# Performance work log

Measured on AMD Instinct MI355X. Metric: run time of the kernel, lower is better.

Reference implementation:

```python
import jax, jax.numpy as jnp
import numpy as np

N, E = 50000, 800000
F_IN, HID, OUT, H = 128, 32, 4, 8
NEG_SLOPE = 0.2


def gat_conv(x, src, dst, W, a_src, a_dst, b):
    """PyG GATConv (concat=True, eval mode). x: [N,Fin]; src/dst: [E'] (self-loops included).
    W: [Fin, Hh*C]; a_src/a_dst: [Hh, C]; b: [Hh*C]."""
    n = x.shape[0]
    Hh, C = a_src.shape
    h = (x @ W).reshape(n, Hh, C)                      # [N,H,C]
    alpha_src = jnp.einsum('nhc,hc->nh', h, a_src)     # [N,H]
    alpha_dst = jnp.einsum('nhc,hc->nh', h, a_dst)     # [N,H]
    alpha = jax.nn.leaky_relu(alpha_src[src] + alpha_dst[dst], NEG_SLOPE)  # [E',H]
    # segment softmax over incoming edges of each dst node
    amax = jax.ops.segment_max(alpha, dst, num_segments=n)  # [N,H]
    ex = jnp.exp(alpha - amax[dst])
    denom = jax.ops.segment_sum(ex, dst, num_segments=n)    # [N,H]
    w = ex / (denom[dst] + 1e-16)                            # [E',H]
    msg = h[src] * w[:, :, None]                             # [E',H,C]
    out = jax.ops.segment_sum(msg, dst, num_segments=n)     # [N,H,C]
    return out.reshape(n, Hh * C) + b


def setup_inputs() -> dict:
    key = jax.random.key(0)
    ks = jax.random.split(key, 9)
    x = jax.random.normal(ks[0], (N, F_IN), jnp.float32)
    # random edge list without self loops (PyG GATConv removes then re-adds self loops)
    rng = np.random.default_rng(0)
    s = rng.integers(0, N, size=E)
    d = rng.integers(0, N, size=E)
    d = np.where(d == s, (d + 1) % N, d)
    edge_index = jnp.asarray(np.stack([s, d]), dtype=jnp.int32)
    g = lambda k, shape, fan: jax.random.normal(k, shape, jnp.float32) * (1.0 / np.sqrt(fan))
    W1 = g(ks[1], (F_IN, H * HID), F_IN)
    a_src1 = g(ks[2], (H, HID), HID)
    a_dst1 = g(ks[3], (H, HID), HID)
    b1 = jnp.zeros((H * HID,), jnp.float32)
    W2 = g(ks[4], (H * HID, H * OUT), H * HID)
    a_src2 = g(ks[5], (H, OUT), OUT)
    a_dst2 = g(ks[6], (H, OUT), OUT)
    b2 = jnp.zeros((H * OUT,), jnp.float32)
    return {"x": x, "edge_index": edge_index, "W1": W1, "a_src1": a_src1,
            "a_dst1": a_dst1, "b1": b1, "W2": W2, "a_src2": a_src2,
            "a_dst2": a_dst2, "b2": b2}


def reference(x, edge_index, W1, a_src1, a_dst1, b1, W2, a_src2, a_dst2, b2):
    n = x.shape[0]
    loops = jnp.arange(n, dtype=edge_index.dtype)
    src = jnp.concatenate([edge_index[0], loops])
    dst = jnp.concatenate([edge_index[1], loops])
    # layer 1 (dropout_edge / dropout are no-ops in eval mode)
    h = gat_conv(x, src, dst, W1, a_src1, a_dst1, b1)
    h = jax.nn.leaky_relu(h, NEG_SLOPE)
    # final layer (concat=True per the original code) -> [N, OUT*H]
    out = gat_conv(h, src, dst, W2, a_src2, a_dst2, b2)
    return out
```

## Files before the change

kernel.cpp:

```cpp
#include <hip/hip_runtime.h>
#include <hip/hip_bf16.h>
#include <cstdint>
#include <cstddef>


__device__ __forceinline__ float lrelu(float a) { return a > 0.f ? a : 0.2f * a; }

__device__ __forceinline__ unsigned short f2bf(float f) {
  unsigned u = __float_as_uint(f);
  unsigned r = (u + 0x7fff + ((u >> 16) & 1)) >> 16;
  return (unsigned short)r;
}
__device__ __forceinline__ float bf_lo(unsigned q) { return __uint_as_float(q << 16); }
__device__ __forceinline__ float bf_hi(unsigned q) { return __uint_as_float(q & 0xffff0000u); }

typedef __attribute__((ext_vector_type(8))) short bf16x8;
typedef __attribute__((ext_vector_type(4))) float f32x4;

#define ROWCAP 64
#define CSTRIDE 16


__global__ __launch_bounds__(256) void k_scatter(const int* __restrict__ srce,
                                                 const int* __restrict__ dste, int E, int n,
                                                 int* __restrict__ cursor,
                                                 int* __restrict__ srcs,
                                                 const float* __restrict__ W1,
                                                 unsigned short* __restrict__ W1T,
                                                 const float* __restrict__ W2,
                                                 unsigned short* __restrict__ W2T,
                                                 const float* __restrict__ as1,
                                                 const float* __restrict__ ad1,
                                                 const float* __restrict__ as2,
                                                 const float* __restrict__ ad2,
                                                 unsigned short* __restrict__ Wa1T,
                                                 unsigned short* __restrict__ Wa2T) {
  int t = blockIdx.x * 256 + threadIdx.x;
  if (t < E + n) {
    int s, d;
    if (t < E) { s = srce[t]; d = dste[t]; } else { s = d = t - E; }
    int pos = atomicAdd(&cursor[d << 4], 1);
    srcs[(d << 6) + pos] = s;
  }
  if (t < 32768) {
    int k = t >> 8;
    int nn = t & 255;
    W1T[nn * 128 + k] = f2bf(W1[k * 256 + nn]);
  }
  if (t < 8192) {
    int k = t >> 5;
    int nn = t & 31;
    W2T[nn * 256 + k] = f2bf(W2[k * 32 + nn]);
  }
  if (t < 2048) {
    int j = t >> 7;
    int k = t & 127;
    const float* av = (j < 8) ? &as1[j * 32] : &ad1[(j - 8) * 32];
    const float* wv = &W1[k * 256 + (j & 7) * 32];
    float s = 0.f;
#pragma unroll
    for (int c = 0; c < 32; c++) s += wv[c] * av[c];
    Wa1T[j * 128 + k] = f2bf(s);
  }
  if (t < 4096) {
    int j = t >> 8;
    int k = t & 255;
    const float* av = (j < 8) ? &as2[j * 4] : &ad2[(j - 8) * 4];
    const float* wv = &W2[k * 32 + (j & 7) * 4];
    float s = 0.f;
#pragma unroll
    for (int c = 0; c < 4; c++) s += wv[c] * av[c];
    Wa2T[j * 256 + k] = f2bf(s);
  }
}


__global__ __launch_bounds__(256) void gemm1_mfma(const float* __restrict__ X,
                                                  const unsigned short* __restrict__ WT,
                                                  const unsigned short* __restrict__ WaT,
                                                  unsigned short* __restrict__ h1,
                                                  float* __restrict__ a_s1,
                                                  float* __restrict__ a_d1,
                                                  int M) {
  __shared__ unsigned short As[64 * 136];
  __shared__ unsigned short Bs[256 * 72];
  __shared__ unsigned short Was[16 * 72];
  const int row0 = blockIdx.x * 64;
  const int tid = threadIdx.x;
  const int wv = tid >> 6, lane = tid & 63;
  const int quad = lane >> 4, l15 = lane & 15;
  const int colw = wv * 64;

#pragma unroll
  for (int i = 0; i < 8; i++) {
    int j = tid + 256 * i;
    int r = j >> 5;
    int c4 = (j & 31) * 4;
    float4 v = make_float4(0.f, 0.f, 0.f, 0.f);
    if (row0 + r < M) v = *(const float4*)&X[(size_t)(row0 + r) * 128 + c4];
    uint2 p;
    p.x = (unsigned)f2bf(v.x) | ((unsigned)f2bf(v.y) << 16);
    p.y = (unsigned)f2bf(v.z) | ((unsigned)f2bf(v.w) << 16);
    *(uint2*)&As[r * 136 + c4] = p;
  }

  f32x4 acc[16];
#pragma unroll
  for (int i = 0; i < 16; i++) acc[i] = (f32x4)0.f;
  f32x4 acca = (f32x4)0.f;

  for (int kc = 0; kc < 128; kc += 64) {
    __syncthreads();
#pragma unroll
    for (int i = 0; i < 8; i++) {
      int j = tid + 256 * i;
      int nn = j >> 3;
      int kg = (j & 7) * 8;
      *(uint4*)&Bs[nn * 72 + kg] = *(const uint4*)&WT[nn * 128 + kc + kg];
    }
    if (tid < 128) {
      int j = tid >> 3;
      int kg = (tid & 7) * 8;
      *(uint4*)&Was[j * 72 + kg] = *(const uint4*)&WaT[j * 128 + kc + kg];
    }
    __syncthreads();
#pragma unroll
    for (int ks = 0; ks < 64; ks += 32) {
      bf16x8 af[4], bfr[4];
#pragma unroll
      for (int mi = 0; mi < 4; mi++)
        af[mi] = *(const bf16x8*)&As[(mi * 16 + l15) * 136 + kc + ks + quad * 8];
#pragma unroll
      for (int ni = 0; ni < 4; ni++)
        bfr[ni] = *(const bf16x8*)&Bs[(colw + ni * 16 + l15) * 72 + ks + quad * 8];
#pragma unroll
      for (int mi = 0; mi < 4; mi++)
#pragma unroll
        for (int ni = 0; ni < 4; ni++)
          acc[mi * 4 + ni] = __builtin_amdgcn_mfma_f32_16x16x32_bf16(
              af[mi], bfr[ni], acc[mi * 4 + ni], 0, 0, 0);
      bf16x8 afa = *(const bf16x8*)&As[(wv * 16 + l15) * 136 + kc + ks + quad * 8];
      bf16x8 bfa = *(const bf16x8*)&Was[l15 * 72 + ks + quad * 8];
      acca = __builtin_amdgcn_mfma_f32_16x16x32_bf16(afa, bfa, acca, 0, 0, 0);
    }
  }

#pragma unroll
  for (int mi = 0; mi < 4; mi++) {
#pragma unroll
    for (int r = 0; r < 4; r++) {
      int m = row0 + mi * 16 + quad * 4 + r;
      if (m < M) {
#pragma unroll
        for (int ni = 0; ni < 4; ni++)
          h1[(size_t)m * 256 + colw + ni * 16 + l15] = f2bf(acc[mi * 4 + ni][r]);
      }
    }
  }
#pragma unroll
  for (int r = 0; r < 4; r++) {
    int m = row0 + wv * 16 + quad * 4 + r;
    if (m < M) {
      if (l15 < 8) a_s1[m * 8 + l15] = acca[r];
      else         a_d1[m * 8 + (l15 - 8)] = acca[r];
    }
  }
}


__global__ __launch_bounds__(256) void gemm2_mfma(const unsigned short* __restrict__ Xb,
                                                  const unsigned short* __restrict__ W2T,
                                                  const unsigned short* __restrict__ WaT,
                                                  unsigned short* __restrict__ h2,
                                                  float* __restrict__ a_s2,
                                                  float* __restrict__ a_d2, int M) {
  __shared__ unsigned short As[64 * 264];
  __shared__ unsigned short Bs[32 * 264];
  __shared__ unsigned short Was[16 * 264];
  const int row0 = blockIdx.x * 64;
  const int tid = threadIdx.x;
  const int wv = tid >> 6, lane = tid & 63;
  const int quad = lane >> 4, l15 = lane & 15;

#pragma unroll
  for (int i = 0; i < 8; i++) {
    int j = tid + 256 * i;
    int r = j >> 5;
    int c8 = (j & 31) * 8;
    uint4 v = make_uint4(0, 0, 0, 0);
    if (row0 + r < M) v = *(const uint4*)&Xb[(size_t)(row0 + r) * 256 + c8];
    *(uint4*)&As[r * 264 + c8] = v;
  }
#pragma unroll
  for (int i = 0; i < 4; i++) {
    int j = tid + 256 * i;
    int nn = j >> 5;
    int kg = (j & 31) * 8;
    *(uint4*)&Bs[nn * 264 + kg] = *(const uint4*)&W2T[nn * 256 + kg];
  }
#pragma unroll
  for (int i = 0; i < 2; i++) {
    int j = tid + 256 * i;
    int nn = j >> 5;
    int kg = (j & 31) * 8;
    *(uint4*)&Was[nn * 264 + kg] = *(const uint4*)&WaT[nn * 256 + kg];
  }
  __syncthreads();

  f32x4 acc[2];
  acc[0] = (f32x4)0.f;
  acc[1] = (f32x4)0.f;
  f32x4 acca = (f32x4)0.f;
  const int mr = wv * 16;
#pragma unroll
  for (int ks = 0; ks < 256; ks += 32) {
    bf16x8 af = *(const bf16x8*)&As[(mr + l15) * 264 + ks + quad * 8];
    bf16x8 b0 = *(const bf16x8*)&Bs[(l15) * 264 + ks + quad * 8];
    bf16x8 b1 = *(const bf16x8*)&Bs[(16 + l15) * 264 + ks + quad * 8];
    bf16x8 ba = *(const bf16x8*)&Was[(l15) * 264 + ks + quad * 8];
    acc[0] = __builtin_amdgcn_mfma_f32_16x16x32_bf16(af, b0, acc[0], 0, 0, 0);
    acc[1] = __builtin_amdgcn_mfma_f32_16x16x32_bf16(af, b1, acc[1], 0, 0, 0);
    acca   = __builtin_amdgcn_mfma_f32_16x16x32_bf16(af, ba, acca, 0, 0, 0);
  }

#pragma unroll
  for (int r = 0; r < 4; r++) {
    int m = row0 + mr + quad * 4 + r;
    if (m < M) {
      h2[(size_t)m * 32 + l15]      = f2bf(acc[0][r]);
      h2[(size_t)m * 32 + 16 + l15] = f2bf(acc[1][r]);
      if (l15 < 8) a_s2[m * 8 + l15] = acca[r];
      else         a_d2[m * 8 + (l15 - 8)] = acca[r];
    }
  }
}


__global__ __launch_bounds__(256) void gat_agg_l1(const unsigned short* __restrict__ h,
                                                  const float* __restrict__ asrc,
                                                  const float* __restrict__ adst,
                                                  const int* __restrict__ rowcnt,
                                                  const int* __restrict__ srcs,
                                                  const float* __restrict__ bias,
                                                  unsigned short* __restrict__ out, int n) {
  int wave = threadIdx.x >> 6;
  int lane = threadIdx.x & 63;
  int d = blockIdx.x * 4 + wave;
  if (d >= n) return;
  d = __builtin_amdgcn_readfirstlane(d);
  const int cnt = __builtin_amdgcn_readfirstlane(rowcnt[d << 4]);
  const int* __restrict__ row = srcs + (d << 6);
  const int myhead = lane >> 3;
  float ad = adst[d * 8 + myhead];

  float denom = 0.f;
  float4 acc0 = make_float4(0.f, 0.f, 0.f, 0.f);
  float4 acc1 = make_float4(0.f, 0.f, 0.f, 0.f);
#define ACCA(ff, qq)                                        \
    acc0.x = fmaf(ff, bf_lo(qq.x), acc0.x);                 \
    acc0.y = fmaf(ff, bf_hi(qq.x), acc0.y);                 \
    acc0.z = fmaf(ff, bf_lo(qq.y), acc0.z);                 \
    acc0.w = fmaf(ff, bf_hi(qq.y), acc0.w);
#define ACCB(ff, qq)                                        \
    acc1.x = fmaf(ff, bf_lo(qq.x), acc1.x);                 \
    acc1.y = fmaf(ff, bf_hi(qq.x), acc1.y);                 \
    acc1.z = fmaf(ff, bf_lo(qq.y), acc1.z);                 \
    acc1.w = fmaf(ff, bf_hi(qq.y), acc1.w);

  for (int e = 0; e < cnt; e += 12) {
    int s[12];
#pragma unroll
    for (int j = 0; j < 12; j++) {
      int ee = e + j;
      s[j] = __builtin_amdgcn_readfirstlane(row[ee < cnt ? ee : cnt - 1]);
    }
    uint2 q[12];
#pragma unroll
    for (int j = 0; j < 12; j++)
      q[j] = *(const uint2*)&h[(size_t)s[j] * 256 + lane * 4];
    float av[12];
#pragma unroll
    for (int j = 0; j < 12; j++) av[j] = asrc[s[j] * 8 + myhead];
#pragma unroll
    for (int j = 0; j < 12; j += 2) {
      float w0 = (e + j     < cnt) ? __expf(lrelu(av[j]     + ad)) : 0.f;
      float w1 = (e + j + 1 < cnt) ? __expf(lrelu(av[j + 1] + ad)) : 0.f;
      denom += w0 + w1;
      ACCA(w0, q[j])
      ACCB(w1, q[j + 1])
    }
  }
#undef ACCA
#undef ACCB
  float4 acc;
  acc.x = acc0.x + acc1.x;
  acc.y = acc0.y + acc1.y;
  acc.z = acc0.z + acc1.z;
  acc.w = acc0.w + acc1.w;
  float inv = 1.f / (denom + 1e-16f);
  int f = lane * 4;
  float4 bv = *(const float4*)&bias[f];
  float rx = lrelu(acc.x * inv + bv.x);
  float ry = lrelu(acc.y * inv + bv.y);
  float rz = lrelu(acc.z * inv + bv.z);
  float rw = lrelu(acc.w * inv + bv.w);
  uint2 p;
  p.x = (unsigned)f2bf(rx) | ((unsigned)f2bf(ry) << 16);
  p.y = (unsigned)f2bf(rz) | ((unsigned)f2bf(rw) << 16);
  *(uint2*)&out[(size_t)d * 256 + f] = p;
}

__global__ __launch_bounds__(256) void gat_agg_l2(const unsigned short* __restrict__ h,
                                                  const float* __restrict__ asrc,
                                                  const float* __restrict__ adst,
                                                  const int* __restrict__ rowcnt,
                                                  const int* __restrict__ srcs,
                                                  const float* __restrict__ bias,
                                                  float* __restrict__ out, int n) {
  int wave = threadIdx.x >> 6;
  int lane = threadIdx.x & 63;
  int d = blockIdx.x * 4 + wave;
  if (d >= n) return;
  int begin = d << 6;
  int end = begin + rowcnt[d << 4];
  int hh = lane & 7;
  int eg = lane >> 3;
  float ad = adst[d * 8 + hh];

  float denom = 0.f;
  float4 acc = make_float4(0.f, 0.f, 0.f, 0.f);
  for (int base = begin; base < end; base += 32) {
    int eA = base + eg;
    int eB = base + 8 + eg;
    int eC = base + 16 + eg;
    int eD = base + 24 + eg;
    bool vA = eA < end, vB = eB < end, vC = eC < end, vD = eD < end;
    int sA = srcs[vA ? eA : begin];
    int sB = srcs[vB ? eB : begin];
    int sC = srcs[vC ? eC : begin];
    int sD = srcs[vD ? eD : begin];
    float aA = asrc[sA * 8 + hh];
    float aB = asrc[sB * 8 + hh];
    float aC = asrc[sC * 8 + hh];
    float aD = asrc[sD * 8 + hh];
    uint2 qA = *(const uint2*)&h[(size_t)sA * 32 + hh * 4];
    uint2 qB = *(const uint2*)&h[(size_t)sB * 32 + hh * 4];
    uint2 qC = *(const uint2*)&h[(size_t)sC * 32 + hh * 4];
    uint2 qD = *(const uint2*)&h[(size_t)sD * 32 + hh * 4];
    float wA = vA ? __expf(lrelu(aA + ad)) : 0.f;
    float wB = vB ? __expf(lrelu(aB + ad)) : 0.f;
    float wC = vC ? __expf(lrelu(aC + ad)) : 0.f;
    float wD = vD ? __expf(lrelu(aD + ad)) : 0.f;
    denom += (wA + wB) + (wC + wD);
    acc.x = fmaf(wA, bf_lo(qA.x), acc.x); acc.y = fmaf(wA, bf_hi(qA.x), acc.y);
    acc.z = fmaf(wA, bf_lo(qA.y), acc.z); acc.w = fmaf(wA, bf_hi(qA.y), acc.w);
    acc.x = fmaf(wB, bf_lo(qB.x), acc.x); acc.y = fmaf(wB, bf_hi(qB.x), acc.y);
    acc.z = fmaf(wB, bf_lo(qB.y), acc.z); acc.w = fmaf(wB, bf_hi(qB.y), acc.w);
    acc.x = fmaf(wC, bf_lo(qC.x), acc.x); acc.y = fmaf(wC, bf_hi(qC.x), acc.y);
    acc.z = fmaf(wC, bf_lo(qC.y), acc.z); acc.w = fmaf(wC, bf_hi(qC.y), acc.w);
    acc.x = fmaf(wD, bf_lo(qD.x), acc.x); acc.y = fmaf(wD, bf_hi(qD.x), acc.y);
    acc.z = fmaf(wD, bf_lo(qD.y), acc.z); acc.w = fmaf(wD, bf_hi(qD.y), acc.w);
  }
#pragma unroll
  for (int mask = 8; mask <= 32; mask <<= 1) {
    denom += __shfl_xor(denom, mask);
    acc.x += __shfl_xor(acc.x, mask);
    acc.y += __shfl_xor(acc.y, mask);
    acc.z += __shfl_xor(acc.z, mask);
    acc.w += __shfl_xor(acc.w, mask);
  }
  if (lane < 8) {
    float inv = 1.f / (denom + 1e-16f);
    int f = lane * 4;
    float4 bv = *(const float4*)&bias[f];
    float4 r;
    r.x = acc.x * inv + bv.x;
    r.y = acc.y * inv + bv.y;
    r.z = acc.z * inv + bv.z;
    r.w = acc.w * inv + bv.w;
    *(float4*)&out[(size_t)d * 32 + f] = r;
  }
}


extern "C" void kernel_launch(void* const* d_in, const int* in_sizes, int n_in,
                              void* d_out, int out_size, void* d_ws, size_t ws_size,
                              hipStream_t stream) {
  const float* x   = (const float*)d_in[0];
  const int*   ei  = (const int*)d_in[1];
  const float* W1  = (const float*)d_in[2];
  const float* as1 = (const float*)d_in[3];
  const float* ad1 = (const float*)d_in[4];
  const float* b1  = (const float*)d_in[5];
  const float* W2  = (const float*)d_in[6];
  const float* as2 = (const float*)d_in[7];
  const float* ad2 = (const float*)d_in[8];
  const float* b2  = (const float*)d_in[9];
  float* out = (float*)d_out;

  const int E = in_sizes[1] / 2;
  const int n = in_sizes[0] / 128;
  const int* srce = ei;
  const int* dste = ei + E;

  char* ws = (char*)d_ws;
  size_t off = 0;
  auto alloc = [&](size_t bytes) -> void* {
    void* p = ws + off;
    off = (off + bytes + 255) & ~(size_t)255;
    return p;
  };
  int* cursor   = (int*)alloc((size_t)n * CSTRIDE * 4);
  int* srcs     = (int*)alloc((size_t)n * ROWCAP * 4);
  unsigned short* h1  = (unsigned short*)alloc((size_t)n * 256 * 2);
  unsigned short* w1t = (unsigned short*)alloc((size_t)256 * 128 * 2);
  unsigned short* w2t = (unsigned short*)alloc((size_t)32 * 256 * 2);
  unsigned short* wa1t = (unsigned short*)alloc((size_t)16 * 128 * 2);
  unsigned short* wa2t = (unsigned short*)alloc((size_t)16 * 256 * 2);
  float* a_s1   = (float*)alloc((size_t)n * 8 * 4);
  float* a_d1   = (float*)alloc((size_t)n * 8 * 4);
  unsigned short* x2 = (unsigned short*)alloc((size_t)n * 256 * 2);
  unsigned short* h2 = (unsigned short*)alloc((size_t)n * 32 * 2);
  float* a_s2   = (float*)alloc((size_t)n * 8 * 4);
  float* a_d2   = (float*)alloc((size_t)n * 8 * 4);

  const int tot = E + n;
  hipMemsetAsync(cursor, 0, (size_t)n * CSTRIDE * 4, stream);
  k_scatter<<<(tot + 255) / 256, 256, 0, stream>>>(srce, dste, E, n, cursor, srcs,
                                                   W1, w1t, W2, w2t,
                                                   as1, ad1, as2, ad2, wa1t, wa2t);

  gemm1_mfma<<<(n + 63) / 64, 256, 0, stream>>>(x, w1t, wa1t, h1, a_s1, a_d1, n);
  gat_agg_l1<<<(n + 3) / 4, 256, 0, stream>>>(h1, a_s1, a_d1, cursor, srcs, b1, x2, n);

  gemm2_mfma<<<(n + 63) / 64, 256, 0, stream>>>(x2, w2t, wa2t, h2, a_s2, a_d2, n);
  gat_agg_l2<<<(n + 3) / 4, 256, 0, stream>>>(h2, a_s2, a_d2, cursor, srcs, b2, out, n);
}
```

Baseline: 258.3 us.

## Pre-convert X to bf16 in scatter kernel and read weights directly in gemm1

Moves the fp32-to-bf16 conversion of the input features into the existing scatter/prep kernel, so gemm1 loads compact bf16 rows. gemm1 also drops its shared-memory staging of the weight and attention-projection matrices and reads MFMA B fragments directly from global memory, removing the K-loop barriers and most LDS usage. The trade-off is an extra write and read of the bf16 copy of X, plus relying on cache for the repeated weight fragment loads.

```diff
diff --git a/kernel.cpp b/kernel.cpp
--- a/kernel.cpp
+++ b/kernel.cpp
@@ -25,6 +25,8 @@
                                                  const int* __restrict__ dste, int E, int n,
                                                  int* __restrict__ cursor,
                                                  int* __restrict__ srcs,
+                                                 const float* __restrict__ X,
+                                                 unsigned short* __restrict__ Xb,
                                                  const float* __restrict__ W1,
                                                  unsigned short* __restrict__ W1T,
                                                  const float* __restrict__ W2,
@@ -36,6 +38,21 @@
                                                  unsigned short* __restrict__ Wa1T,
                                                  unsigned short* __restrict__ Wa2T) {
   int t = blockIdx.x * 256 + threadIdx.x;
+
+  {
+    size_t base = (size_t)t * 8;
+    if (base < (size_t)n * 128) {
+      float4 v0 = *(const float4*)&X[base];
+      float4 v1 = *(const float4*)&X[base + 4];
+      uint4 p;
+      p.x = (unsigned)f2bf(v0.x) | ((unsigned)f2bf(v0.y) << 16);
+      p.y = (unsigned)f2bf(v0.z) | ((unsigned)f2bf(v0.w) << 16);
+      p.z = (unsigned)f2bf(v1.x) | ((unsigned)f2bf(v1.y) << 16);
+      p.w = (unsigned)f2bf(v1.z) | ((unsigned)f2bf(v1.w) << 16);
+      *(uint4*)&Xb[base] = p;
+    }
+  }
+
   if (t < E + n) {
     int s, d;
     if (t < E) { s = srce[t]; d = dste[t]; } else { s = d = t - E; }
@@ -75,7 +92,7 @@
 }
 
 
-__global__ __launch_bounds__(256) void gemm1_mfma(const float* __restrict__ X,
+__global__ __launch_bounds__(256) void gemm1_mfma(const unsigned short* __restrict__ Xb,
                                                   const unsigned short* __restrict__ WT,
                                                   const unsigned short* __restrict__ WaT,
                                                   unsigned short* __restrict__ h1,
@@ -83,8 +100,6 @@
                                                   float* __restrict__ a_d1,
                                                   int M) {
   __shared__ unsigned short As[64 * 136];
-  __shared__ unsigned short Bs[256 * 72];
-  __shared__ unsigned short Was[16 * 72];
   const int row0 = blockIdx.x * 64;
   const int tid = threadIdx.x;
   const int wv = tid >> 6, lane = tid & 63;
@@ -92,57 +107,39 @@
   const int colw = wv * 64;
 
 #pragma unroll
-  for (int i = 0; i < 8; i++) {
+  for (int i = 0; i < 4; i++) {
     int j = tid + 256 * i;
-    int r = j >> 5;
-    int c4 = (j & 31) * 4;
-    float4 v = make_float4(0.f, 0.f, 0.f, 0.f);
-    if (row0 + r < M) v = *(const float4*)&X[(size_t)(row0 + r) * 128 + c4];
-    uint2 p;
-    p.x = (unsigned)f2bf(v.x) | ((unsigned)f2bf(v.y) << 16);
-    p.y = (unsigned)f2bf(v.z) | ((unsigned)f2bf(v.w) << 16);
-    *(uint2*)&As[r * 136 + c4] = p;
-  }
+    int r = j >> 4;
+    int c8 = (j & 15) * 8;
+    uint4 v = make_uint4(0, 0, 0, 0);
+    if (row0 + r < M) v = *(const uint4*)&Xb[(size_t)(row0 + r) * 128 + c8];
+    *(uint4*)&As[r * 136 + c8] = v;
+  }
+  __syncthreads();
 
   f32x4 acc[16];
 #pragma unroll
   for (int i = 0; i < 16; i++) acc[i] = (f32x4)0.f;
   f32x4 acca = (f32x4)0.f;
 
-  for (int kc = 0; kc < 128; kc += 64) {
-    __syncthreads();
-#pragma unroll
-    for (int i = 0; i < 8; i++) {
-      int j = tid + 256 * i;
-      int nn = j >> 3;
-      int kg = (j & 7) * 8;
-      *(uint4*)&Bs[nn * 72 + kg] = *(const uint4*)&WT[nn * 128 + kc + kg];
-    }
-    if (tid < 128) {
-      int j = tid >> 3;
-      int kg = (tid & 7) * 8;
-      *(uint4*)&Was[j * 72 + kg] = *(const uint4*)&WaT[j * 128 + kc + kg];
-    }
-    __syncthreads();
-#pragma unroll
-    for (int ks = 0; ks < 64; ks += 32) {
-      bf16x8 af[4], bfr[4];
-#pragma unroll
-      for (int mi = 0; mi < 4; mi++)
-        af[mi] = *(const bf16x8*)&As[(mi * 16 + l15) * 136 + kc + ks + quad * 8];
+#pragma unroll
+  for (int ks = 0; ks < 128; ks += 32) {
+    bf16x8 af[4], bfr[4];
+#pragma unroll
+    for (int mi = 0; mi < 4; mi++)
+      af[mi] = *(const bf16x8*)&As[(mi * 16 + l15) * 136 + ks + quad * 8];
+#pragma unroll
+    for (int ni = 0; ni < 4; ni++)
+      bfr[ni] = *(const bf16x8*)&WT[(size_t)(colw + ni * 16 + l15) * 128 + ks + quad * 8];
+#pragma unroll
+    for (int mi = 0; mi < 4; mi++)
 #pragma unroll
       for (int ni = 0; ni < 4; ni++)
-        bfr[ni] = *(const bf16x8*)&Bs[(colw + ni * 16 + l15) * 72 + ks + quad * 8];
-#pragma unroll
-      for (int mi = 0; mi < 4; mi++)
-#pragma unroll
-        for (int ni = 0; ni < 4; ni++)
-          acc[mi * 4 + ni] = __builtin_amdgcn_mfma_f32_16x16x32_bf16(
-              af[mi], bfr[ni], acc[mi * 4 + ni], 0, 0, 0);
-      bf16x8 afa = *(const bf16x8*)&As[(wv * 16 + l15) * 136 + kc + ks + quad * 8];
-      bf16x8 bfa = *(const bf16x8*)&Was[l15 * 72 + ks + quad * 8];
-      acca = __builtin_amdgcn_mfma_f32_16x16x32_bf16(afa, bfa, acca, 0, 0, 0);
-    }
+        acc[mi * 4 + ni] = __builtin_amdgcn_mfma_f32_16x16x32_bf16(
+            af[mi], bfr[ni], acc[mi * 4 + ni], 0, 0, 0);
+    bf16x8 afa = *(const bf16x8*)&As[(wv * 16 + l15) * 136 + ks + quad * 8];
+    bf16x8 bfa = *(const bf16x8*)&WaT[l15 * 128 + ks + quad * 8];
+    acca = __builtin_amdgcn_mfma_f32_16x16x32_bf16(afa, bfa, acca, 0, 0, 0);
   }
 
 #pragma unroll
@@ -412,6 +409,7 @@
   };
   int* cursor   = (int*)alloc((size_t)n * CSTRIDE * 4);
   int* srcs     = (int*)alloc((size_t)n * ROWCAP * 4);
+  unsigned short* xb  = (unsigned short*)alloc((size_t)n * 128 * 2);
   unsigned short* h1  = (unsigned short*)alloc((size_t)n * 256 * 2);
   unsigned short* w1t = (unsigned short*)alloc((size_t)256 * 128 * 2);
   unsigned short* w2t = (unsigned short*)alloc((size_t)32 * 256 * 2);
@@ -427,10 +425,10 @@
   const int tot = E + n;
   hipMemsetAsync(cursor, 0, (size_t)n * CSTRIDE * 4, stream);
   k_scatter<<<(tot + 255) / 256, 256, 0, stream>>>(srce, dste, E, n, cursor, srcs,
-                                                   W1, w1t, W2, w2t,
+                                                   x, xb, W1, w1t, W2, w2t,
                                                    as1, ad1, as2, ad2, wa1t, wa2t);
 
-  gemm1_mfma<<<(n + 63) / 64, 256, 0, stream>>>(x, w1t, wa1t, h1, a_s1, a_d1, n);
+  gemm1_mfma<<<(n + 63) / 64, 256, 0, stream>>>(xb, w1t, wa1t, h1, a_s1, a_d1, n);
   gat_agg_l1<<<(n + 3) / 4, 256, 0, stream>>>(h1, a_s1, a_d1, cursor, srcs, b1, x2, n);
 
   gemm2_mfma<<<(n + 63) / 64, 256, 0, stream>>>(x2, w2t, wa2t, h2, a_s2, a_d2, n);
```

Result: no change. 258.3 us (-0.0%).

## Fuse edge scatter into GEMM1 launch and read weights directly from global

Applied to the files above, without the earlier changes.

The edge-bucketing scatter moves out of the weight-prep kernel into extra blocks of the first GEMM launch, so the atomic-heavy scatter and the MFMA GEMM can run concurrently on different CUs. Weight transposition now runs in a small separate prep kernel of 128 blocks. The GEMM also drops its LDS staging of the weight tiles and loads B fragments straight from global memory (L2-resident), which removes the extra syncs and LDS traffic. The cost is an additional kernel launch and uncoalesced, repeated global loads of the weights.

```diff
diff --git a/kernel.cpp b/kernel.cpp
--- a/kernel.cpp
+++ b/kernel.cpp
@@ -21,27 +21,17 @@
 #define CSTRIDE 16
 
 
-__global__ __launch_bounds__(256) void k_scatter(const int* __restrict__ srce,
-                                                 const int* __restrict__ dste, int E, int n,
-                                                 int* __restrict__ cursor,
-                                                 int* __restrict__ srcs,
-                                                 const float* __restrict__ W1,
-                                                 unsigned short* __restrict__ W1T,
-                                                 const float* __restrict__ W2,
-                                                 unsigned short* __restrict__ W2T,
-                                                 const float* __restrict__ as1,
-                                                 const float* __restrict__ ad1,
-                                                 const float* __restrict__ as2,
-                                                 const float* __restrict__ ad2,
-                                                 unsigned short* __restrict__ Wa1T,
-                                                 unsigned short* __restrict__ Wa2T) {
+__global__ __launch_bounds__(256) void k_prep(const float* __restrict__ W1,
+                                              unsigned short* __restrict__ W1T,
+                                              const float* __restrict__ W2,
+                                              unsigned short* __restrict__ W2T,
+                                              const float* __restrict__ as1,
+                                              const float* __restrict__ ad1,
+                                              const float* __restrict__ as2,
+                                              const float* __restrict__ ad2,
+                                              unsigned short* __restrict__ Wa1T,
+                                              unsigned short* __restrict__ Wa2T) {
   int t = blockIdx.x * 256 + threadIdx.x;
-  if (t < E + n) {
-    int s, d;
-    if (t < E) { s = srce[t]; d = dste[t]; } else { s = d = t - E; }
-    int pos = atomicAdd(&cursor[d << 4], 1);
-    srcs[(d << 6) + pos] = s;
-  }
   if (t < 32768) {
     int k = t >> 8;
     int nn = t & 255;
@@ -75,17 +65,32 @@
 }
 
 
-__global__ __launch_bounds__(256) void gemm1_mfma(const float* __restrict__ X,
-                                                  const unsigned short* __restrict__ WT,
-                                                  const unsigned short* __restrict__ WaT,
-                                                  unsigned short* __restrict__ h1,
-                                                  float* __restrict__ a_s1,
-                                                  float* __restrict__ a_d1,
-                                                  int M) {
+__global__ __launch_bounds__(256) void fused_front(const float* __restrict__ X,
+                                                   const unsigned short* __restrict__ WT,
+                                                   const unsigned short* __restrict__ WaT,
+                                                   unsigned short* __restrict__ h1,
+                                                   float* __restrict__ a_s1,
+                                                   float* __restrict__ a_d1,
+                                                   int M,
+                                                   const int* __restrict__ srce,
+                                                   const int* __restrict__ dste, int E,
+                                                   int* __restrict__ cursor,
+                                                   int* __restrict__ srcs,
+                                                   int SB) {
   __shared__ unsigned short As[64 * 136];
-  __shared__ unsigned short Bs[256 * 72];
-  __shared__ unsigned short Was[16 * 72];
-  const int row0 = blockIdx.x * 64;
+
+  if ((int)blockIdx.x < SB) {
+    int t = blockIdx.x * 256 + threadIdx.x;
+    if (t < E + M) {
+      int s, d;
+      if (t < E) { s = srce[t]; d = dste[t]; } else { s = d = t - E; }
+      int pos = atomicAdd(&cursor[d << 4], 1);
+      srcs[(d << 6) + pos] = s;
+    }
+    return;
+  }
+
+  const int row0 = ((int)blockIdx.x - SB) * 64;
   const int tid = threadIdx.x;
   const int wv = tid >> 6, lane = tid & 63;
   const int quad = lane >> 4, l15 = lane & 15;
@@ -103,46 +108,31 @@
     p.y = (unsigned)f2bf(v.z) | ((unsigned)f2bf(v.w) << 16);
     *(uint2*)&As[r * 136 + c4] = p;
   }
+  __syncthreads();
 
   f32x4 acc[16];
 #pragma unroll
   for (int i = 0; i < 16; i++) acc[i] = (f32x4)0.f;
   f32x4 acca = (f32x4)0.f;
 
-  for (int kc = 0; kc < 128; kc += 64) {
-    __syncthreads();
-#pragma unroll
-    for (int i = 0; i < 8; i++) {
-      int j = tid + 256 * i;
-      int nn = j >> 3;
-      int kg = (j & 7) * 8;
-      *(uint4*)&Bs[nn * 72 + kg] = *(const uint4*)&WT[nn * 128 + kc + kg];
-    }
-    if (tid < 128) {
-      int j = tid >> 3;
-      int kg = (tid & 7) * 8;
-      *(uint4*)&Was[j * 72 + kg] = *(const uint4*)&WaT[j * 128 + kc + kg];
-    }
-    __syncthreads();
-#pragma unroll
-    for (int ks = 0; ks < 64; ks += 32) {
-      bf16x8 af[4], bfr[4];
-#pragma unroll
-      for (int mi = 0; mi < 4; mi++)
-        af[mi] = *(const bf16x8*)&As[(mi * 16 + l15) * 136 + kc + ks + quad * 8];
+#pragma unroll
+  for (int ks = 0; ks < 128; ks += 32) {
+    bf16x8 af[4], bfr[4];
+#pragma unroll
+    for (int mi = 0; mi < 4; mi++)
+      af[mi] = *(const bf16x8*)&As[(mi * 16 + l15) * 136 + ks + quad * 8];
+#pragma unroll
+    for (int ni = 0; ni < 4; ni++)
+      bfr[ni] = *(const bf16x8*)&WT[(size_t)(colw + ni * 16 + l15) * 128 + ks + quad * 8];
+#pragma unroll
+    for (int mi = 0; mi < 4; mi++)
 #pragma unroll
       for (int ni = 0; ni < 4; ni++)
-        bfr[ni] = *(const bf16x8*)&Bs[(colw + ni * 16 + l15) * 72 + ks + quad * 8];
-#pragma unroll
-      for (int mi = 0; mi < 4; mi++)
-#pragma unroll
-        for (int ni = 0; ni < 4; ni++)
-          acc[mi * 4 + ni] = __builtin_amdgcn_mfma_f32_16x16x32_bf16(
-              af[mi], bfr[ni], acc[mi * 4 + ni], 0, 0, 0);
-      bf16x8 afa = *(const bf16x8*)&As[(wv * 16 + l15) * 136 + kc + ks + quad * 8];
-      bf16x8 bfa = *(const bf16x8*)&Was[l15 * 72 + ks + quad * 8];
-      acca = __builtin_amdgcn_mfma_f32_16x16x32_bf16(afa, bfa, acca, 0, 0, 0);
-    }
+        acc[mi * 4 + ni] = __builtin_amdgcn_mfma_f32_16x16x32_bf16(
+            af[mi], bfr[ni], acc[mi * 4 + ni], 0, 0, 0);
+    bf16x8 afa = *(const bf16x8*)&As[(wv * 16 + l15) * 136 + ks + quad * 8];
+    bf16x8 bfa = *(const bf16x8*)&WaT[l15 * 128 + ks + quad * 8];
+    acca = __builtin_amdgcn_mfma_f32_16x16x32_bf16(afa, bfa, acca, 0, 0, 0);
   }
 
 #pragma unroll
@@ -424,13 +414,15 @@
   float* a_s2   = (float*)alloc((size_t)n * 8 * 4);
   float* a_d2   = (float*)alloc((size_t)n * 8 * 4);
 
-  const int tot = E + n;
+  const int SB = (E + n + 255) / 256;
+  const int GB = (n + 63) / 64;
+
   hipMemsetAsync(cursor, 0, (size_t)n * CSTRIDE * 4, stream);
-  k_scatter<<<(tot + 255) / 256, 256, 0, stream>>>(srce, dste, E, n, cursor, srcs,
-                                                   W1, w1t, W2, w2t,
-                                                   as1, ad1, as2, ad2, wa1t, wa2t);
-
-  gemm1_mfma<<<(n + 63) / 64, 256, 0, stream>>>(x, w1t, wa1t, h1, a_s1, a_d1, n);
+  k_prep<<<128, 256, 0, stream>>>(W1, w1t, W2, w2t, as1, ad1, as2, ad2, wa1t, wa2t);
+
+  fused_front<<<SB + GB, 256, 0, stream>>>(x, w1t, wa1t, h1, a_s1, a_d1, n,
+                                           srce, dste, E, cursor, srcs, SB);
+
   gat_agg_l1<<<(n + 3) / 4, 256, 0, stream>>>(h1, a_s1, a_d1, cursor, srcs, b1, x2, n);
 
   gemm2_mfma<<<(n + 63) / 64, 256, 0, stream>>>(x2, w2t, wa2t, h2, a_s2, a_d2, n);
```

Result: slower. 286.0 us (+10.7%).
